# Kernel optimization log

Hardware: AMD Instinct MI355X
Metric: run time of the kernel (lower is better)

## Reference

```python
import jax, jax.numpy as jnp
import numpy as np

B, S, E, H = 2, 2048, 2048, 16
D = E // H  # head_dim = 128
ROPE_BASE = 10000.0


def _rope_tables(seq_len, dim, dtype):
    inv_freq = 1.0 / (ROPE_BASE ** (jnp.arange(0, dim, 2, dtype=jnp.float32) / dim))
    pos = jnp.arange(seq_len, dtype=jnp.float32)
    freqs = jnp.outer(pos, inv_freq)            # [S, D/2]
    emb = jnp.concatenate([freqs, freqs], -1)    # [S, D]
    return jnp.cos(emb).astype(dtype), jnp.sin(emb).astype(dtype)


def _rotate_half(x):
    x1, x2 = jnp.split(x, 2, axis=-1)
    return jnp.concatenate([-x2, x1], axis=-1)


def _apply_rope(x, cos, sin):
    # x: [B,H,S,D]; cos/sin: [S,D] broadcast over batch+heads
    return x * cos[None, None] + _rotate_half(x) * sin[None, None]


def setup_inputs() -> dict:
    key = jax.random.key(0)
    k1, k2, k3 = jax.random.split(key, 3)
    x = jax.random.normal(k1, (B, S, E), dtype=jnp.float32)
    w_qkv = jax.random.normal(k2, (3 * E, E), dtype=jnp.float32) * (E ** -0.5)
    w_out = jax.random.normal(k3, (E, E), dtype=jnp.float32) * (E ** -0.5)
    return {"x": x, "w_qkv": w_qkv, "w_out": w_out}


def reference(x, w_qkv, w_out):
    b, s, e = x.shape
    qkv = x @ w_qkv.T                                # [B,S,3E]
    q, k, v = jnp.split(qkv, 3, axis=-1)
    def to_heads(t):
        return t.reshape(b, s, H, D).transpose(0, 2, 1, 3)  # [B,H,S,D]
    q, k, v = to_heads(q), to_heads(k), to_heads(v)
    cos, sin = _rope_tables(s, D, x.dtype)
    q = _apply_rope(q, cos, sin)
    k = _apply_rope(k, cos, sin)
    scale = 1.0 / jnp.sqrt(jnp.asarray(D, x.dtype))
    scores = jnp.einsum('bhqd,bhkd->bhqk', q, k) * scale
    causal = jnp.tril(jnp.ones((s, s), dtype=bool))
    scores = jnp.where(causal[None, None], scores, jnp.asarray(-jnp.inf, scores.dtype))
    attn = jax.nn.softmax(scores, axis=-1)
    y = jnp.einsum('bhqk,bhkd->bhqd', attn, v)       # [B,H,S,D]
    y = y.transpose(0, 2, 1, 3).reshape(b, s, e)
    return y @ w_out.T
```

## Files before the change

### kernel.cpp

```cpp
#include <hip/hip_runtime.h>
#include <stdint.h>

constexpr int BATCH = 2;
constexpr int SEQ   = 2048;
constexpr int EMB   = 2048;
constexpr int NH    = 16;
constexpr int HD    = 128;
constexpr int QKV3  = 3 * EMB;

typedef unsigned short u16;
typedef __attribute__((ext_vector_type(8))) short bf16x8;
typedef __attribute__((ext_vector_type(4))) float floatx4;

__device__ inline float bf2f(u16 u) {
  union { unsigned int i; float f; } v; v.i = ((unsigned int)u) << 16; return v.f;
}
__device__ inline u16 f2bf(float f) {
  union { float f; unsigned int i; } v; v.f = f;
  unsigned int x = v.i;
  return (u16)((x + 0x7fffu + ((x >> 16) & 1u)) >> 16);
}

__device__ inline void load_lds16(const void* g, void* l) {
  __builtin_amdgcn_global_load_lds((const __attribute__((address_space(1))) unsigned int*)g,
                                   (__attribute__((address_space(3))) unsigned int*)l,
                                   16, 0, 0);
}

__device__ inline void block_barrier() {
  __builtin_amdgcn_sched_barrier(0);
  asm volatile("" ::: "memory");
  __builtin_amdgcn_s_barrier();
  asm volatile("" ::: "memory");
  __builtin_amdgcn_sched_barrier(0);
}

__global__ void cvt_f32_bf16(const float* __restrict__ src, u16* __restrict__ dst, int n4) {
  const int i = blockIdx.x * blockDim.x + threadIdx.x;
  if (i < n4) {
    const float4 v = ((const float4*)src)[i];
    ushort4 o;
    o.x = f2bf(v.x); o.y = f2bf(v.y); o.z = f2bf(v.z); o.w = f2bf(v.w);
    ((ushort4*)dst)[i] = o;
  }
}

constexpr int BM = 128, BN = 128, BK = 32;

template <bool F32OUT>
__global__ __launch_bounds__(256) void gemm_bt(const u16* __restrict__ A,
                                               const u16* __restrict__ Bm,
                                               u16* __restrict__ Cb,
                                               float* __restrict__ Cf,
                                               int M, int N, int K) {
  __shared__ __align__(16) u16 As[BM * BK];
  __shared__ __align__(16) u16 Bs[BN * BK];
  const int tid  = threadIdx.x;
  const int wave = tid >> 6, lane = tid & 63;
  const int wm = (wave & 1) * 64, wn = (wave >> 1) * 64;
  const int m0 = blockIdx.y * BM, n0 = blockIdx.x * BN;

  floatx4 acc[4][4];
#pragma unroll
  for (int i = 0; i < 4; ++i)
#pragma unroll
    for (int j = 0; j < 4; ++j) acc[i][j] = {0.f, 0.f, 0.f, 0.f};

  const int lrow = lane >> 2;
  const int lcol = (lane & 3) * 8;
  const int frow = lane & 15;
  const int fk   = (lane >> 4) * 8;

  for (int kt = 0; kt < K; kt += BK) {
#pragma unroll
    for (int inst = 0; inst < 2; ++inst) {
      const int rbase = wave * 32 + inst * 16;
      load_lds16(A  + (size_t)(m0 + rbase + lrow) * K + kt + lcol, &As[rbase * BK]);
      load_lds16(Bm + (size_t)(n0 + rbase + lrow) * K + kt + lcol, &Bs[rbase * BK]);
    }
    asm volatile("s_waitcnt vmcnt(0)" ::: "memory");
    __syncthreads();

    bf16x8 af[4], bfr[4];
#pragma unroll
    for (int mi = 0; mi < 4; ++mi)
      af[mi] = *(const bf16x8*)&As[(wm + mi * 16 + frow) * BK + fk];
#pragma unroll
    for (int ni = 0; ni < 4; ++ni)
      bfr[ni] = *(const bf16x8*)&Bs[(wn + ni * 16 + frow) * BK + fk];
#pragma unroll
    for (int mi = 0; mi < 4; ++mi)
#pragma unroll
      for (int ni = 0; ni < 4; ++ni)
        acc[mi][ni] = __builtin_amdgcn_mfma_f32_16x16x32_bf16(af[mi], bfr[ni], acc[mi][ni], 0, 0, 0);
    __syncthreads();
  }

  const int crow0 = (lane >> 4) * 4;
  const int ccol  = lane & 15;
#pragma unroll
  for (int mi = 0; mi < 4; ++mi)
#pragma unroll
    for (int ni = 0; ni < 4; ++ni) {
      const int row = m0 + wm + mi * 16 + crow0;
      const int col = n0 + wn + ni * 16 + ccol;
#pragma unroll
      for (int r = 0; r < 4; ++r) {
        const size_t off = (size_t)(row + r) * N + col;
        if (F32OUT) Cf[off] = acc[mi][ni][r];
        else        Cb[off] = f2bf(acc[mi][ni][r]);
      }
    }
}

__global__ __launch_bounds__(512, 2) void gemm_bt256(const u16* __restrict__ A,
                                                     const u16* __restrict__ Bm,
                                                     u16* __restrict__ Cb,
                                                     int M, int N, int K) {
  __shared__ __align__(16) u16 sh2[65536];
  char* ldsb = (char*)sh2;

  const int tid  = threadIdx.x;
  const int wave = tid >> 6, lane = tid & 63;
  const int wr = wave >> 2;
  const int wc = wave & 3;
  const int m0 = blockIdx.y * 256, n0 = blockIdx.x * 256;
  const int frow = lane & 15, quad = lane >> 4;

  const int KT = K >> 6;

  auto stage = [&](int t, int d) {
    const int r_lo = lane >> 3;
    const int colE = (((lane & 7) ^ r_lo) << 3);
#pragma unroll
    for (int hf = 0; hf < 4; ++hf) {
      const u16* src = (hf < 2) ? (A + (size_t)(m0 + hf * 128) * K)
                                : (Bm + (size_t)(n0 + (hf - 2) * 128) * K);
#pragma unroll
      for (int j = 0; j < 2; ++j) {
        const int r = (wave * 2 + j) * 8 + r_lo;
        load_lds16(src + (size_t)r * K + t * 64 + colE,
                   ldsb + d * 65536 + hf * 16384 + (wave * 2 + j) * 1024);
      }
    }
  };

  floatx4 acc[8][4];
#pragma unroll
  for (int i = 0; i < 8; ++i)
#pragma unroll
    for (int j = 0; j < 4; ++j) acc[i][j] = {0.f, 0.f, 0.f, 0.f};

  stage(0, 0);
  stage(1, 1);

  for (int t = 0; t < KT; ++t) {
    if (t + 1 < KT) asm volatile("s_waitcnt vmcnt(8)" ::: "memory");
    else            asm volatile("s_waitcnt vmcnt(0)" ::: "memory");
    block_barrier();

    const char* abuf = ldsb + (t & 1) * 65536 + wr * 16384;
    const char* bbuf = ldsb + (t & 1) * 65536 + 32768 + (wc >> 1) * 16384;

    bf16x8 bfr[4][2];
#pragma unroll
    for (int ni = 0; ni < 4; ++ni) {
      const int rb = (wc & 1) * 64 + ni * 16 + frow;
#pragma unroll
      for (int kk = 0; kk < 2; ++kk) {
        const int cb = (kk * 64 + quad * 16) ^ ((rb & 7) << 4);
        bfr[ni][kk] = *(const bf16x8*)(bbuf + rb * 128 + cb);
      }
    }
    bf16x8 af[4][2];
#pragma unroll
    for (int mi = 0; mi < 4; ++mi) {
      const int ra = mi * 16 + frow;
#pragma unroll
      for (int kk = 0; kk < 2; ++kk) {
        const int cb = (kk * 64 + quad * 16) ^ ((ra & 7) << 4);
        af[mi][kk] = *(const bf16x8*)(abuf + ra * 128 + cb);
      }
    }
    asm volatile("s_waitcnt lgkmcnt(0)" ::: "memory");
    __builtin_amdgcn_sched_barrier(0);

    __builtin_amdgcn_s_setprio(1);
#pragma unroll
    for (int mi = 0; mi < 4; ++mi)
#pragma unroll
      for (int ni = 0; ni < 4; ++ni)
#pragma unroll
        for (int kk = 0; kk < 2; ++kk)
          acc[mi][ni] = __builtin_amdgcn_mfma_f32_16x16x32_bf16(af[mi][kk], bfr[ni][kk], acc[mi][ni], 0, 0, 0);
    __builtin_amdgcn_s_setprio(0);

#pragma unroll
    for (int mi = 0; mi < 4; ++mi) {
      const int ra = 64 + mi * 16 + frow;
#pragma unroll
      for (int kk = 0; kk < 2; ++kk) {
        const int cb = (kk * 64 + quad * 16) ^ ((ra & 7) << 4);
        af[mi][kk] = *(const bf16x8*)(abuf + ra * 128 + cb);
      }
    }
    asm volatile("s_waitcnt lgkmcnt(0)" ::: "memory");
    __builtin_amdgcn_sched_barrier(0);
    block_barrier();

    if (t + 2 < KT) stage(t + 2, t & 1);

    __builtin_amdgcn_s_setprio(1);
#pragma unroll
    for (int mi = 0; mi < 4; ++mi)
#pragma unroll
      for (int ni = 0; ni < 4; ++ni)
#pragma unroll
        for (int kk = 0; kk < 2; ++kk)
          acc[4 + mi][ni] = __builtin_amdgcn_mfma_f32_16x16x32_bf16(af[mi][kk], bfr[ni][kk], acc[4 + mi][ni], 0, 0, 0);
    __builtin_amdgcn_s_setprio(0);
  }

#pragma unroll
  for (int mi = 0; mi < 8; ++mi)
#pragma unroll
    for (int ni = 0; ni < 4; ++ni) {
      const int row = m0 + wr * 128 + mi * 16 + quad * 4;
      const int col = n0 + wc * 64 + ni * 16 + frow;
#pragma unroll
      for (int r = 0; r < 4; ++r)
        Cb[(size_t)(row + r) * N + col] = f2bf(acc[mi][ni][r]);
    }
}

__global__ void rope_inplace(u16* __restrict__ qkv) {
  const int t   = blockIdx.x * blockDim.x + threadIdx.x;
  const int j   = t & 63;
  const int idx = t >> 6;
  const int h   = idx & (NH - 1);
  const int bs  = idx >> 4;
  const int s   = bs & (SEQ - 1);

  u16* base = qkv + (size_t)bs * QKV3 + h * HD;

  const float inv_freq = exp2f(-(float)j * (13.287712379549449f / 64.0f));
  const float ang = (float)s * inv_freq;
  const float c = cosf(ang), sn = sinf(ang);

#pragma unroll
  for (int part = 0; part < 2; ++part) {
    u16* p = base + part * EMB;
    const float x1 = bf2f(p[j]), x2 = bf2f(p[j + 64]);
    p[j]      = f2bf(x1 * c - x2 * sn);
    p[j + 64] = f2bf(x2 * c + x1 * sn);
  }
}

__global__ __launch_bounds__(256) void transpose_v(const u16* __restrict__ qkv,
                                                   u16* __restrict__ VT) {
  __shared__ u16 vtile[64][136];
  const int tid = threadIdx.x;
  const int s0 = blockIdx.x * 64;
  const int bh = blockIdx.y;
  const int b = bh >> 4, h = bh & 15;

  const u16* Vp = qkv + (size_t)b * SEQ * QKV3 + 2 * EMB + h * HD;
  {
    const int r = tid >> 2, cp = (tid & 3) * 32;
    const uint4* src = (const uint4*)(Vp + (size_t)(s0 + r) * QKV3 + cp);
    uint4* dst = (uint4*)&vtile[r][cp];
    dst[0] = src[0]; dst[1] = src[1]; dst[2] = src[2]; dst[3] = src[3];
  }
  __syncthreads();
  {
    const int d = tid >> 1, ck = (tid & 1) * 32;
    ushort4 o[8];
#pragma unroll
    for (int i = 0; i < 8; ++i) {
      o[i].x = vtile[ck + i * 4 + 0][d];
      o[i].y = vtile[ck + i * 4 + 1][d];
      o[i].z = vtile[ck + i * 4 + 2][d];
      o[i].w = vtile[ck + i * 4 + 3][d];
    }
    ushort4* dst = (ushort4*)(VT + ((size_t)bh * HD + d) * SEQ + s0 + ck);
#pragma unroll
    for (int i = 0; i < 8; ++i) dst[i] = o[i];
  }
}

constexpr int PSTR = 72;

__global__ __launch_bounds__(256, 2) void attn_mfma(const u16* __restrict__ qkv,
                                                    const u16* __restrict__ VT,
                                                    u16* __restrict__ Y) {
  __shared__ __align__(16) u16 kb[2][64 * 128];
  __shared__ __align__(16) u16 vb[128 * 64];
  __shared__ __align__(16) u16 p_sh[4][32][PSTR];

  const int tid  = threadIdx.x;
  const int wave = tid >> 6, lane = tid & 63;
  const int bid  = blockIdx.x;
  const int bh   = bid & 31;
  const int pc   = bid >> 5;
  const int cq   = (pc < 8) ? pc : 23 - pc;
  const int qa   = cq;
  const int qb   = 31 - cq;
  const int b = bh >> 4, h = bh & 15;

  const u16* Qp  = qkv + (size_t)b * SEQ * QKV3 + h * HD;
  const u16* Kp  = Qp + EMB;
  const u16* VTp = VT + (size_t)bh * HD * SEQ;

  const int NT = 32 - cq;

  u16* kbf = &kb[0][0];

  {
    const int rl  = lane >> 4;
    const int cbp = (lane & 15) * 16;
#pragma unroll
    for (int i = 0; i < 8; ++i) {
      const int cc = wave * 8 + i;
      const int r  = cc * 4 + rl;
      const int gq = (r < 64) ? (qa * 64 + r) : (qb * 64 + r - 64);
      const int cbl = cbp ^ ((r & 7) << 4);
      load_lds16(Qp + (size_t)gq * QKV3 + (cbl >> 1), kbf + cc * 512);
    }
  }
  asm volatile("s_waitcnt vmcnt(0)" ::: "memory");
  block_barrier();

  const int frow = lane & 15;
  const int quad = lane >> 4;

  bf16x8 aq[2][4];
#pragma unroll
  for (int m = 0; m < 2; ++m)
#pragma unroll
    for (int ks = 0; ks < 4; ++ks) {
      const int qr = m * 64 + wave * 16 + frow;
      const int cb = (ks * 64 + quad * 16) ^ ((qr & 7) << 4);
      aq[m][ks] = *(const bf16x8*)((const char*)kbf + qr * 256 + cb);
    }
  asm volatile("s_waitcnt lgkmcnt(0)" ::: "memory");
  block_barrier();

  auto stage_k = [&](int t, int sel) {
    const int rl  = lane >> 4;
    const int cbp = (lane & 15) * 16;
#pragma unroll
    for (int i = 0; i < 4; ++i) {
      const int cc = wave * 4 + i;
      const int r  = cc * 4 + rl;
      const int cbl = cbp ^ ((r & 7) << 4);
      load_lds16(Kp + (size_t)(t * 64 + r) * QKV3 + (cbl >> 1), &kb[sel][cc * 512]);
    }
  };
  auto stage_v = [&](int t) {
    const int rl  = lane >> 3;
    const int cbp = (lane & 7) * 16;
#pragma unroll
    for (int i = 0; i < 4; ++i) {
      const int cc = wave * 4 + i;
      const int r  = cc * 8 + rl;
      const int cbl = cbp ^ ((r & 7) << 4);
      load_lds16(VTp + (size_t)r * SEQ + t * 64 + (cbl >> 1), vb + cc * 512);
    }
  };

  floatx4 o_acc[2][8];
#pragma unroll
  for (int m = 0; m < 2; ++m)
#pragma unroll
    for (int dt = 0; dt < 8; ++dt) o_acc[m][dt] = {0.f, 0.f, 0.f, 0.f};
  float m_r[2][4], l_r[2][4];
#pragma unroll
  for (int m = 0; m < 2; ++m)
#pragma unroll
    for (int r = 0; r < 4; ++r) { m_r[m][r] = -INFINITY; l_r[m][r] = 0.f; }

  const float scale = 0.08838834764831845f;
  const float THR   = 90.50966799187809f;

  stage_k(0, 0);

  for (int t = 0; t < NT; ++t) {
    block_barrier();
    stage_v(t);
    const bool havek = (t + 1 < NT);
    if (havek) stage_k(t + 1, (t + 1) & 1);
    if (havek) asm volatile("s_waitcnt vmcnt(8)" ::: "memory");
    else       asm volatile("s_waitcnt vmcnt(4)" ::: "memory");
    block_barrier();

    const char* kbuf = (const char*)&kb[t & 1][0];
    const bool aAct = (t <= qa);

    floatx4 s4[2][4];
    __builtin_amdgcn_s_setprio(1);
    if (aAct) {
#pragma unroll
      for (int nt = 0; nt < 4; ++nt) {
        floatx4 a0 = {0.f, 0.f, 0.f, 0.f}, a1 = {0.f, 0.f, 0.f, 0.f};
#pragma unroll
        for (int ks = 0; ks < 4; ++ks) {
          const int kr = nt * 16 + frow;
          const int cb = (ks * 64 + quad * 16) ^ ((kr & 7) << 4);
          const bf16x8 bk = *(const bf16x8*)(kbuf + kr * 256 + cb);
          a0 = __builtin_amdgcn_mfma_f32_16x16x32_bf16(aq[0][ks], bk, a0, 0, 0, 0);
          a1 = __builtin_amdgcn_mfma_f32_16x16x32_bf16(aq[1][ks], bk, a1, 0, 0, 0);
        }
        s4[0][nt] = a0; s4[1][nt] = a1;
      }
    } else {
#pragma unroll
      for (int nt = 0; nt < 4; ++nt) {
        floatx4 a1 = {0.f, 0.f, 0.f, 0.f};
#pragma unroll
        for (int ks = 0; ks < 4; ++ks) {
          const int kr = nt * 16 + frow;
          const int cb = (ks * 64 + quad * 16) ^ ((kr & 7) << 4);
          const bf16x8 bk = *(const bf16x8*)(kbuf + kr * 256 + cb);
          a1 = __builtin_amdgcn_mfma_f32_16x16x32_bf16(aq[1][ks], bk, a1, 0, 0, 0);
        }
        s4[1][nt] = a1;
      }
    }
    __builtin_amdgcn_s_setprio(0);

#pragma unroll
    for (int m = 0; m < 2; ++m) {
      if (m == 0 && !aAct) continue;
      const int tdiag = (m == 0) ? qa : qb;
      if (t == tdiag) {
#pragma unroll
        for (int nt = 0; nt < 4; ++nt)
#pragma unroll
          for (int r = 0; r < 4; ++r) {
            const int key = t * 64 + nt * 16 + frow;
            const int qg  = tdiag * 64 + wave * 16 + quad * 4 + r;
            if (key > qg) s4[m][nt][r] = -INFINITY;
          }
      }
      float mt[4];
#pragma unroll
      for (int r = 0; r < 4; ++r)
        mt[r] = fmaxf(fmaxf(s4[m][0][r], s4[m][1][r]), fmaxf(s4[m][2][r], s4[m][3][r]));
#pragma unroll
      for (int off = 1; off <= 8; off <<= 1)
#pragma unroll
        for (int r = 0; r < 4; ++r) mt[r] = fmaxf(mt[r], __shfl_xor(mt[r], off));

      bool grow = false;
#pragma unroll
      for (int r = 0; r < 4; ++r) grow = grow || (mt[r] > m_r[m][r] + THR);
      if (__any((int)grow)) {
#pragma unroll
        for (int r = 0; r < 4; ++r) {
          const float mnew  = fmaxf(m_r[m][r], mt[r]);
          const float alpha = __expf((m_r[m][r] - mnew) * scale);
          m_r[m][r] = mnew;
          l_r[m][r] *= alpha;
#pragma unroll
          for (int dt = 0; dt < 8; ++dt) o_acc[m][dt][r] *= alpha;
        }
      }

      float rs[4] = {0.f, 0.f, 0.f, 0.f};
#pragma unroll
      for (int nt = 0; nt < 4; ++nt)
#pragma unroll
        for (int r = 0; r < 4; ++r) {
          const float pp = __expf((s4[m][nt][r] - m_r[m][r]) * scale);
          s4[m][nt][r] = pp;
          rs[r] += pp;
        }
#pragma unroll
      for (int off = 1; off <= 8; off <<= 1)
#pragma unroll
        for (int r = 0; r < 4; ++r) rs[r] += __shfl_xor(rs[r], off);
#pragma unroll
      for (int r = 0; r < 4; ++r) l_r[m][r] += rs[r];
    }

    if (havek) asm volatile("s_waitcnt vmcnt(4)" ::: "memory");
    else       asm volatile("s_waitcnt vmcnt(0)" ::: "memory");
    block_barrier();

#pragma unroll
    for (int m = 0; m < 2; ++m) {
      if (m == 0 && !aAct) continue;
#pragma unroll
      for (int nt = 0; nt < 4; ++nt)
#pragma unroll
        for (int r = 0; r < 4; ++r)
          p_sh[wave][m * 16 + quad * 4 + r][nt * 16 + frow] = f2bf(s4[m][nt][r]);
    }
    __builtin_amdgcn_s_setprio(1);
    if (aAct) {
#pragma unroll
      for (int step = 0; step < 2; ++step) {
        const bf16x8 ap0 = *(const bf16x8*)&p_sh[wave][frow]     [step * 32 + quad * 8];
        const bf16x8 ap1 = *(const bf16x8*)&p_sh[wave][16 + frow][step * 32 + quad * 8];
#pragma unroll
        for (int dt = 0; dt < 8; ++dt) {
          const int vr = dt * 16 + frow;
          const int cb = (step * 64 + quad * 16) ^ ((vr & 7) << 4);
          const bf16x8 bv = *(const bf16x8*)((const char*)vb + vr * 128 + cb);
          o_acc[0][dt] = __builtin_amdgcn_mfma_f32_16x16x32_bf16(ap0, bv, o_acc[0][dt], 0, 0, 0);
          o_acc[1][dt] = __builtin_amdgcn_mfma_f32_16x16x32_bf16(ap1, bv, o_acc[1][dt], 0, 0, 0);
        }
      }
    } else {
#pragma unroll
      for (int step = 0; step < 2; ++step) {
        const bf16x8 ap1 = *(const bf16x8*)&p_sh[wave][16 + frow][step * 32 + quad * 8];
#pragma unroll
        for (int dt = 0; dt < 8; ++dt) {
          const int vr = dt * 16 + frow;
          const int cb = (step * 64 + quad * 16) ^ ((vr & 7) << 4);
          const bf16x8 bv = *(const bf16x8*)((const char*)vb + vr * 128 + cb);
          o_acc[1][dt] = __builtin_amdgcn_mfma_f32_16x16x32_bf16(ap1, bv, o_acc[1][dt], 0, 0, 0);
        }
      }
    }
    __builtin_amdgcn_s_setprio(0);
  }

#pragma unroll
  for (int m = 0; m < 2; ++m) {
    const int qbase = ((m == 0) ? qa : qb) * 64 + wave * 16;
    float invl[4];
#pragma unroll
    for (int r = 0; r < 4; ++r) invl[r] = 1.f / l_r[m][r];
#pragma unroll
    for (int dt = 0; dt < 8; ++dt)
#pragma unroll
      for (int r = 0; r < 4; ++r) {
        const int qg = qbase + quad * 4 + r;
        const size_t off = ((size_t)b * SEQ + qg) * EMB + h * HD + dt * 16 + frow;
        Y[off] = f2bf(o_acc[m][dt][r] * invl[r]);
      }
  }
}

extern "C" void kernel_launch(void* const* d_in, const int* in_sizes, int n_in,
                              void* d_out, int out_size, void* d_ws, size_t ws_size,
                              hipStream_t stream) {
  const float* x_f     = (const float*)d_in[0];
  const float* w_qkv_f = (const float*)d_in[1];
  const float* w_out_f = (const float*)d_in[2];
  float* out = (float*)d_out;

  const int M = BATCH * SEQ;
  const size_t n_x    = (size_t)M * EMB;
  const size_t n_wqkv = (size_t)3 * EMB * EMB;
  const size_t n_wout = (size_t)EMB * EMB;

  u16* xb    = (u16*)d_ws;
  u16* wqkvb = xb + n_x;
  u16* qkv   = wqkvb + n_wqkv;
  u16* VT    = qkv + (size_t)M * QKV3;
  u16* woutb = wqkvb;
  u16* Yb    = xb;

  cvt_f32_bf16<<<(int)((n_x / 4 + 255) / 256), 256, 0, stream>>>(x_f, xb, (int)(n_x / 4));
  cvt_f32_bf16<<<(int)((n_wqkv / 4 + 255) / 256), 256, 0, stream>>>(w_qkv_f, wqkvb, (int)(n_wqkv / 4));

  gemm_bt256<<<dim3(QKV3 / 256, M / 256), 512, 0, stream>>>(
      xb, wqkvb, qkv, M, QKV3, EMB);

  rope_inplace<<<(BATCH * SEQ * NH * 64) / 256, 256, 0, stream>>>(qkv);
  transpose_v<<<dim3(SEQ / 64, BATCH * NH), 256, 0, stream>>>(qkv, VT);

  cvt_f32_bf16<<<(int)((n_wout / 4 + 255) / 256), 256, 0, stream>>>(w_out_f, woutb, (int)(n_wout / 4));

  attn_mfma<<<dim3((SEQ / 128) * BATCH * NH), 256, 0, stream>>>(qkv, VT, Yb);

  gemm_bt<true><<<dim3(EMB / BN, M / BM), 256, 0, stream>>>(
      Yb, woutb, nullptr, out, M, EMB, EMB);
}
```

Measured before the change: 432.1 us.

## Use 256x192 tiles with interleaved staged prefetch in the QKV GEMM

Changes the QKV projection GEMM tile from 256x256 to 256x192 and remaps the 8 waves to a 4x2 grid, each computing 64x96. Grid width grows from 24 to 32 column tiles, giving 512 blocks instead of 384 on the device's CUs to improve wave quantization. The pipeline goes from two-ahead staging to one-ahead double buffering, with the next tile's loads split across three MFMA phases. The exchange is more block barriers per k-step and lower arithmetic intensity per block.

Measured after the change: 417.4 us. -3.4%, faster.

```diff
diff --git a/kernel.cpp b/kernel.cpp
--- a/kernel.cpp
+++ b/kernel.cpp
@@ -113,120 +113,147 @@
     }
 }
 
-__global__ __launch_bounds__(512, 2) void gemm_bt256(const u16* __restrict__ A,
+__global__ __launch_bounds__(512, 2) void gemm_bt192(const u16* __restrict__ A,
                                                      const u16* __restrict__ Bm,
                                                      u16* __restrict__ Cb,
                                                      int M, int N, int K) {
-  __shared__ __align__(16) u16 sh2[65536];
-  char* ldsb = (char*)sh2;
+  __shared__ __align__(16) u16 sh[57344];
+  char* ldsb = (char*)sh;
 
   const int tid  = threadIdx.x;
   const int wave = tid >> 6, lane = tid & 63;
-  const int wr = wave >> 2;
-  const int wc = wave & 3;
-  const int m0 = blockIdx.y * 256, n0 = blockIdx.x * 256;
+  const int wrow = wave >> 1;
+  const int wcol = wave & 1;
+  const int m0 = blockIdx.y * 256, n0 = blockIdx.x * 192;
   const int frow = lane & 15, quad = lane >> 4;
-
   const int KT = K >> 6;
 
-  auto stage = [&](int t, int d) {
-    const int r_lo = lane >> 3;
-    const int colE = (((lane & 7) ^ r_lo) << 3);
-#pragma unroll
-    for (int hf = 0; hf < 4; ++hf) {
-      const u16* src = (hf < 2) ? (A + (size_t)(m0 + hf * 128) * K)
-                                : (Bm + (size_t)(n0 + (hf - 2) * 128) * K);
-#pragma unroll
-      for (int j = 0; j < 2; ++j) {
-        const int r = (wave * 2 + j) * 8 + r_lo;
-        load_lds16(src + (size_t)r * K + t * 64 + colE,
-                   ldsb + d * 65536 + hf * 16384 + (wave * 2 + j) * 1024);
-      }
-    }
+  const int srow8 = tid >> 3;
+  const int scolE = (((tid & 7) ^ (srow8 & 7)) << 3);
+  auto stageA = [&](int t, int d, int a) {
+    const int r = a * 64 + srow8;
+    load_lds16(A + (size_t)(m0 + r) * K + t * 64 + scolE,
+               ldsb + d * 57344 + a * 8192 + wave * 1024);
   };
-
-  floatx4 acc[8][4];
-#pragma unroll
-  for (int i = 0; i < 8; ++i)
-#pragma unroll
-    for (int j = 0; j < 4; ++j) acc[i][j] = {0.f, 0.f, 0.f, 0.f};
-
-  stage(0, 0);
-  stage(1, 1);
+  auto stageB = [&](int t, int d, int bi) {
+    const int r = bi * 64 + srow8;
+    load_lds16(Bm + (size_t)(n0 + r) * K + t * 64 + scolE,
+               ldsb + d * 57344 + 32768 + bi * 8192 + wave * 1024);
+  };
+
+  floatx4 acc[4][6];
+#pragma unroll
+  for (int i = 0; i < 4; ++i)
+#pragma unroll
+    for (int j = 0; j < 6; ++j) acc[i][j] = {0.f, 0.f, 0.f, 0.f};
+
+#pragma unroll
+  for (int a = 0; a < 4; ++a) stageA(0, 0, a);
+#pragma unroll
+  for (int bi = 0; bi < 3; ++bi) stageB(0, 0, bi);
 
   for (int t = 0; t < KT; ++t) {
-    if (t + 1 < KT) asm volatile("s_waitcnt vmcnt(8)" ::: "memory");
-    else            asm volatile("s_waitcnt vmcnt(0)" ::: "memory");
-    block_barrier();
-
-    const char* abuf = ldsb + (t & 1) * 65536 + wr * 16384;
-    const char* bbuf = ldsb + (t & 1) * 65536 + 32768 + (wc >> 1) * 16384;
-
-    bf16x8 bfr[4][2];
-#pragma unroll
-    for (int ni = 0; ni < 4; ++ni) {
-      const int rb = (wc & 1) * 64 + ni * 16 + frow;
+    const int d = t & 1, dn = d ^ 1;
+    const char* dbuf = ldsb + d * 57344;
+    const bool pf = (t + 1 < KT);
+
+    if (pf) {
+      stageA(t + 1, dn, 0); stageA(t + 1, dn, 1); stageA(t + 1, dn, 2);
+      asm volatile("s_waitcnt vmcnt(3)" ::: "memory");
+    } else {
+      asm volatile("s_waitcnt vmcnt(0)" ::: "memory");
+    }
+    block_barrier();
+
+    bf16x8 af[4][2], bf0[2][2];
+#pragma unroll
+    for (int mi = 0; mi < 4; ++mi) {
+      const int ra = wrow * 64 + mi * 16 + frow;
+#pragma unroll
+      for (int kk = 0; kk < 2; ++kk) {
+        const int cb = (kk * 64 + quad * 16) ^ ((ra & 7) << 4);
+        af[mi][kk] = *(const bf16x8*)(dbuf + ra * 128 + cb);
+      }
+    }
+#pragma unroll
+    for (int ni = 0; ni < 2; ++ni) {
+      const int rb = wcol * 96 + ni * 16 + frow;
 #pragma unroll
       for (int kk = 0; kk < 2; ++kk) {
         const int cb = (kk * 64 + quad * 16) ^ ((rb & 7) << 4);
-        bfr[ni][kk] = *(const bf16x8*)(bbuf + rb * 128 + cb);
-      }
-    }
-    bf16x8 af[4][2];
-#pragma unroll
-    for (int mi = 0; mi < 4; ++mi) {
-      const int ra = mi * 16 + frow;
-#pragma unroll
-      for (int kk = 0; kk < 2; ++kk) {
-        const int cb = (kk * 64 + quad * 16) ^ ((ra & 7) << 4);
-        af[mi][kk] = *(const bf16x8*)(abuf + ra * 128 + cb);
+        bf0[ni][kk] = *(const bf16x8*)(dbuf + 32768 + rb * 128 + cb);
       }
     }
     asm volatile("s_waitcnt lgkmcnt(0)" ::: "memory");
     __builtin_amdgcn_sched_barrier(0);
-
     __builtin_amdgcn_s_setprio(1);
 #pragma unroll
     for (int mi = 0; mi < 4; ++mi)
 #pragma unroll
-      for (int ni = 0; ni < 4; ++ni)
+      for (int ni = 0; ni < 2; ++ni)
 #pragma unroll
         for (int kk = 0; kk < 2; ++kk)
-          acc[mi][ni] = __builtin_amdgcn_mfma_f32_16x16x32_bf16(af[mi][kk], bfr[ni][kk], acc[mi][ni], 0, 0, 0);
+          acc[mi][ni] = __builtin_amdgcn_mfma_f32_16x16x32_bf16(af[mi][kk], bf0[ni][kk], acc[mi][ni], 0, 0, 0);
     __builtin_amdgcn_s_setprio(0);
-
-#pragma unroll
-    for (int mi = 0; mi < 4; ++mi) {
-      const int ra = 64 + mi * 16 + frow;
+    block_barrier();
+
+    bf16x8 bf1[2][2];
+#pragma unroll
+    for (int ni = 0; ni < 2; ++ni) {
+      const int rb = wcol * 96 + (2 + ni) * 16 + frow;
 #pragma unroll
       for (int kk = 0; kk < 2; ++kk) {
-        const int cb = (kk * 64 + quad * 16) ^ ((ra & 7) << 4);
-        af[mi][kk] = *(const bf16x8*)(abuf + ra * 128 + cb);
-      }
-    }
+        const int cb = (kk * 64 + quad * 16) ^ ((rb & 7) << 4);
+        bf1[ni][kk] = *(const bf16x8*)(dbuf + 32768 + rb * 128 + cb);
+      }
+    }
+    if (pf) { stageA(t + 1, dn, 3); stageB(t + 1, dn, 0); }
+    block_barrier();
     asm volatile("s_waitcnt lgkmcnt(0)" ::: "memory");
     __builtin_amdgcn_sched_barrier(0);
-    block_barrier();
-
-    if (t + 2 < KT) stage(t + 2, t & 1);
-
     __builtin_amdgcn_s_setprio(1);
 #pragma unroll
     for (int mi = 0; mi < 4; ++mi)
 #pragma unroll
-      for (int ni = 0; ni < 4; ++ni)
+      for (int ni = 0; ni < 2; ++ni)
 #pragma unroll
         for (int kk = 0; kk < 2; ++kk)
-          acc[4 + mi][ni] = __builtin_amdgcn_mfma_f32_16x16x32_bf16(af[mi][kk], bfr[ni][kk], acc[4 + mi][ni], 0, 0, 0);
+          acc[mi][2 + ni] = __builtin_amdgcn_mfma_f32_16x16x32_bf16(af[mi][kk], bf1[ni][kk], acc[mi][2 + ni], 0, 0, 0);
     __builtin_amdgcn_s_setprio(0);
-  }
-
-#pragma unroll
-  for (int mi = 0; mi < 8; ++mi)
-#pragma unroll
-    for (int ni = 0; ni < 4; ++ni) {
-      const int row = m0 + wr * 128 + mi * 16 + quad * 4;
-      const int col = n0 + wc * 64 + ni * 16 + frow;
+    block_barrier();
+
+    bf16x8 bf2[2][2];
+#pragma unroll
+    for (int ni = 0; ni < 2; ++ni) {
+      const int rb = wcol * 96 + (4 + ni) * 16 + frow;
+#pragma unroll
+      for (int kk = 0; kk < 2; ++kk) {
+        const int cb = (kk * 64 + quad * 16) ^ ((rb & 7) << 4);
+        bf2[ni][kk] = *(const bf16x8*)(dbuf + 32768 + rb * 128 + cb);
+      }
+    }
+    if (pf) { stageB(t + 1, dn, 1); stageB(t + 1, dn, 2); }
+    block_barrier();
+    asm volatile("s_waitcnt lgkmcnt(0)" ::: "memory");
+    __builtin_amdgcn_sched_barrier(0);
+    __builtin_amdgcn_s_setprio(1);
+#pragma unroll
+    for (int mi = 0; mi < 4; ++mi)
+#pragma unroll
+      for (int ni = 0; ni < 2; ++ni)
+#pragma unroll
+        for (int kk = 0; kk < 2; ++kk)
+          acc[mi][4 + ni] = __builtin_amdgcn_mfma_f32_16x16x32_bf16(af[mi][kk], bf2[ni][kk], acc[mi][4 + ni], 0, 0, 0);
+    __builtin_amdgcn_s_setprio(0);
+    block_barrier();
+  }
+
+#pragma unroll
+  for (int mi = 0; mi < 4; ++mi)
+#pragma unroll
+    for (int ni = 0; ni < 6; ++ni) {
+      const int row = m0 + wrow * 64 + mi * 16 + quad * 4;
+      const int col = n0 + wcol * 96 + ni * 16 + frow;
 #pragma unroll
       for (int r = 0; r < 4; ++r)
         Cb[(size_t)(row + r) * N + col] = f2bf(acc[mi][ni][r]);
@@ -567,7 +594,7 @@
   cvt_f32_bf16<<<(int)((n_x / 4 + 255) / 256), 256, 0, stream>>>(x_f, xb, (int)(n_x / 4));
   cvt_f32_bf16<<<(int)((n_wqkv / 4 + 255) / 256), 256, 0, stream>>>(w_qkv_f, wqkvb, (int)(n_wqkv / 4));
 
-  gemm_bt256<<<dim3(QKV3 / 256, M / 256), 512, 0, stream>>>(
+  gemm_bt192<<<dim3(QKV3 / 192, M / 256), 512, 0, stream>>>(
       xb, wqkvb, qkv, M, QKV3, EMB);
 
   rope_inplace<<<(BATCH * SEQ * NH * 64) / 256, 256, 0, stream>>>(qkv);
```
